# Kernel optimization log

Hardware: AMD Instinct MI355X
Metric: run time of the kernel (lower is better)

## Reference

```python
import jax, jax.numpy as jnp
import numpy as np

K = 2048      # codebook_size
D = 64        # codebook_dim
B = 32
T = 4096
W = 0.99      # codebook_loss_weight (EMA decay)
THRESH = 1.0  # discard_vec_threshold


def setup_inputs() -> dict:
    key = jax.random.key(0)
    k1, k2 = jax.random.split(key, 2)
    x = jax.random.normal(k1, (B, D, T), jnp.float32)
    codebook = jax.random.normal(k2, (K, D), jnp.float32)
    codebook_avg = codebook.copy()
    vector_usage = jnp.ones((K,), jnp.float32)
    perm = jnp.arange(B * T, dtype=jnp.int32)  # deterministic stand-in for randperm
    return dict(x=x, codebook=codebook, codebook_avg=codebook_avg,
                vector_usage=vector_usage, perm=perm)


def reference(x, codebook, codebook_avg, vector_usage, perm):
    Bv, E, Tv = x.shape
    sg = jax.lax.stop_gradient
    # preprocess: [B, E, T] -> [N, E]
    xf = jnp.transpose(x, (0, 2, 1)).reshape(-1, E)
    N = xf.shape[0]
    x_norm = jnp.linalg.norm(xf - jnp.mean(xf)) / np.sqrt(N * E)
    # squared euclidean distances [N, K]
    d = (jnp.sum(xf * xf, axis=-1, keepdims=True)
         - 2.0 * (xf @ codebook.T)
         + jnp.sum(codebook * codebook, axis=-1))
    idx = jnp.argmin(d, axis=-1)            # [N]
    fit = jnp.mean(jnp.min(d, axis=-1))
    q = codebook[idx]                       # [N, E] gather
    # --- update_codebook (torch.no_grad) ---
    cb_sum = jax.ops.segment_sum(sg(xf), idx, num_segments=K)          # onehot @ x
    counts = jax.ops.segment_sum(jnp.ones((N,), xf.dtype), idx, num_segments=K)
    new_avg = W * sg(codebook_avg) + (1.0 - W) * cb_sum
    new_usage = W * sg(vector_usage) + (1.0 - W) * counts
    keep = (new_usage >= THRESH).astype(xf.dtype)[:, None]
    random_shift = sg(xf)[perm][:K]
    new_codebook = keep * (new_avg / new_usage[:, None]) + (1.0 - keep) * random_shift
    vector_prob = counts / jnp.sum(counts)
    entropy = -jnp.sum(vector_prob * jnp.log(vector_prob + 1e-8))
    codebook_diff = jnp.linalg.norm(new_codebook - sg(codebook)) / np.sqrt(K * E)
    # --- commitment loss + straight-through ---
    commit_loss = jnp.sum((sg(q) - xf) ** 2) / (N * E)
    out = xf + sg(q - xf)
    out = jnp.transpose(out.reshape(Bv, Tv, E), (0, 2, 1))  # [B, E, T]
    return (out, commit_loss, fit, x_norm, new_codebook, new_avg, new_usage,
            entropy, codebook_diff)
```

## Files before the change

### kernel.cpp

```cpp
#include <hip/hip_runtime.h>
#include <math.h>

#define OUT_X      0
#define OUT_COMMIT 8388608
#define OUT_FIT    8388609
#define OUT_XNORM  8388610
#define OUT_NCB    8388611
#define OUT_NAVG   (8388611 + 131072)
#define OUT_NUSE   (8388611 + 262144)
#define OUT_ENT    (8388611 + 264192)
#define OUT_CBDIFF (8388611 + 264193)

#define WS_DACC    0
#define WS_COUNTS  64
#define WS_CBSUM   8256
#define WS_CURS    532544
#define WS_XN2     540736
#define WS_IDX     1065024
#define WS_CN2H    1589312
#define WS_SORTED  1597504
#define WS_CHI     2121792
#define WS_CLO     2383936
#define WS_ZERO_BYTES 532544

#define LO_SCALE   2048.0f
#define LO_INV     4.8828125e-4f

typedef _Float16 f16x8_t __attribute__((ext_vector_type(8)));
typedef float f32x16_t __attribute__((ext_vector_type(16)));

__device__ __forceinline__ void gload_lds16(const _Float16* g, _Float16* l) {
    __builtin_amdgcn_global_load_lds(
        (const __attribute__((address_space(1))) unsigned int*)(g),
        (__attribute__((address_space(3))) unsigned int*)(l), 16, 0, 0);
}

__global__ __launch_bounds__(256) void kern_prep_x(
    const float* __restrict__ x, float* __restrict__ xt,
    float* __restrict__ xn2, double* __restrict__ dacc)
{
    __shared__ __align__(16) float Xs[64][128];
    __shared__ float tmpA[4], tmpB[4];
    const int tid = threadIdx.x;
    const int n0 = blockIdx.x * 128;
    const int b = n0 >> 12, t0 = n0 & 4095;
    const float* xb = x + ((size_t)b << 18) + t0;
#pragma unroll
    for (int i = 0; i < 8; ++i) {
        int c = i * 256 + tid;
        int e = c >> 5, v4 = c & 31;
        float4 f = *(const float4*)(xb + ((size_t)e << 12) + (v4 << 2));
        *(float4*)&Xs[e][v4 << 2] = f;
    }
    __syncthreads();
    const int q = tid & 3, r0 = tid >> 2;
    float s1t = 0.f, s2t = 0.f;
#pragma unroll
    for (int h = 0; h < 2; ++h) {
        int r = r0 + (h << 6);
        float s2 = 0.f;
#pragma unroll
        for (int j = 0; j < 4; ++j) {
            int e = q * 16 + j * 4;
            float4 f = make_float4(Xs[e][r], Xs[e + 1][r], Xs[e + 2][r], Xs[e + 3][r]);
            *(float4*)(xt + (((size_t)(n0 + r)) << 6) + e) = f;
            s1t += f.x + f.y + f.z + f.w;
            s2 += f.x * f.x + f.y * f.y + f.z * f.z + f.w * f.w;
        }
        s2t += s2;
        float s2q = s2 + __shfl_xor(s2, 1, 64);
        s2q += __shfl_xor(s2q, 2, 64);
        if (q == 0) xn2[n0 + r] = s2q;
    }
    float rs = s1t, r2 = s2t;
#pragma unroll
    for (int m = 32; m >= 1; m >>= 1) {
        rs += __shfl_xor(rs, m, 64);
        r2 += __shfl_xor(r2, m, 64);
    }
    if ((tid & 63) == 0) { tmpA[tid >> 6] = rs; tmpB[tid >> 6] = r2; }
    __syncthreads();
    if (tid == 0) {
        atomicAdd(&dacc[0], (double)(tmpA[0] + tmpA[1] + tmpA[2] + tmpA[3]));
        atomicAdd(&dacc[1], (double)(tmpB[0] + tmpB[1] + tmpB[2] + tmpB[3]));
    }
}

__global__ __launch_bounds__(256) void kern_prep_cb(
    const float* __restrict__ cb, _Float16* __restrict__ chi,
    _Float16* __restrict__ clo, float* __restrict__ cn2h)
{
    __shared__ float Cs[128][68];
    const int tid = threadIdx.x;
    const int c0 = blockIdx.x * 128;
#pragma unroll
    for (int i = 0; i < 8; ++i) {
        int li = i * 256 + tid;
        int code = li >> 4, d4 = li & 15;
        float4 f = *(const float4*)(cb + (((size_t)(c0 + code)) << 6) + (d4 << 2));
        Cs[code][d4 * 4 + 0] = f.x; Cs[code][d4 * 4 + 1] = f.y;
        Cs[code][d4 * 4 + 2] = f.z; Cs[code][d4 * 4 + 3] = f.w;
    }
    __syncthreads();
    const int w = tid >> 6, lane = tid & 63;
    const int cl = (w << 5) + (lane & 31);
    const int g = lane >> 5;
    const int ktg = blockIdx.x * 4 + w;
#pragma unroll
    for (int s = 0; s < 4; ++s) {
        f16x8_t hh, ll;
#pragma unroll
        for (int i = 0; i < 8; ++i) {
            int k = 16 * s + 4 * g + (i & 3) + 8 * (i >> 2);
            float v = Cs[cl][k];
            _Float16 h = (_Float16)v;
            hh[i] = h;
            ll[i] = (_Float16)((v - (float)h) * LO_SCALE);
        }
        *(f16x8_t*)(chi + (((size_t)(ktg * 4 + s)) << 9) + lane * 8) = hh;
        *(f16x8_t*)(clo + (((size_t)(ktg * 4 + s)) << 9) + lane * 8) = ll;
    }
    if (tid < 128) {
        float s = 0.f;
#pragma unroll
        for (int k = 0; k < 64; ++k) { float v = Cs[tid][k]; s = fmaf(v, v, s); }
        cn2h[c0 + tid] = -0.5f * s;
    }
}

__global__ __launch_bounds__(256, 4) void kern_argmin_mfma(
    const float* __restrict__ xt, const float* __restrict__ cn2h,
    const _Float16* __restrict__ chi, const _Float16* __restrict__ clo,
    const float* __restrict__ xn2, int* __restrict__ idxb,
    unsigned* __restrict__ counts, double* __restrict__ dacc)
{
    __shared__ __align__(16) _Float16 Bs[2][2][8][512];
    const int tid = threadIdx.x;
    const int w = tid >> 6, lane = tid & 63;
    const int n0 = blockIdx.x * 128 + w * 32;
    const int l31 = lane & 31, g = lane >> 5;

    f16x8_t ahi[4], alo[4];
    {
        const float* xr = xt + ((size_t)(n0 + l31) << 6) + 4 * g;
#pragma unroll
        for (int s = 0; s < 4; ++s) {
            float4 p = *(const float4*)(xr + 16 * s);
            float4 q = *(const float4*)(xr + 16 * s + 8);
            float vals[8] = {p.x, p.y, p.z, p.w, q.x, q.y, q.z, q.w};
#pragma unroll
            for (int i = 0; i < 8; ++i) {
                _Float16 h = (_Float16)vals[i];
                ahi[s][i] = h;
                alo[s][i] = (_Float16)((vals[i] - (float)h) * LO_SCALE);
            }
        }
    }
    float bestm[16]; int besti[16];
#pragma unroll
    for (int r = 0; r < 16; ++r) { bestm[r] = -INFINITY; besti[r] = 0; }

#pragma unroll
    for (int j = 0; j < 4; ++j) {
        int seg = (j << 2) | w;
        int tt = seg >> 3, sh = seg & 7;
        size_t off = (((size_t)(0 * 2 + tt) * 4 + (sh >> 1)) << 9) + lane * 8;
        gload_lds16(((sh & 1) ? clo : chi) + off, &Bs[0][tt][sh][0]);
    }
    __syncthreads();
    int buf = 0;
    for (int kt2 = 0; kt2 < 32; ++kt2) {
        if (kt2 + 1 < 32) {
#pragma unroll
            for (int j = 0; j < 4; ++j) {
                int seg = (j << 2) | w;
                int tt = seg >> 3, sh = seg & 7;
                size_t off = (((size_t)(kt2 + 1) * 2 + tt) * 4 + (sh >> 1) << 9) + lane * 8;
                gload_lds16(((sh & 1) ? clo : chi) + off, &Bs[buf ^ 1][tt][sh][0]);
            }
        }
#pragma unroll
        for (int tt = 0; tt < 2; ++tt) {
            const int tg = kt2 * 2 + tt;
            float cv = cn2h[(tg << 5) + l31];
            f32x16_t am, ac;
#pragma unroll
            for (int r = 0; r < 16; ++r) { am[r] = cv; ac[r] = 0.f; }
#pragma unroll
            for (int s = 0; s < 4; ++s) {
                f16x8_t bh = *(const f16x8_t*)&Bs[buf][tt][s * 2 + 0][lane * 8];
                f16x8_t bl = *(const f16x8_t*)&Bs[buf][tt][s * 2 + 1][lane * 8];
                ac = __builtin_amdgcn_mfma_f32_32x32x16_f16(alo[s], bh, ac, 0, 0, 0);
                ac = __builtin_amdgcn_mfma_f32_32x32x16_f16(ahi[s], bl, ac, 0, 0, 0);
                am = __builtin_amdgcn_mfma_f32_32x32x16_f16(ahi[s], bh, am, 0, 0, 0);
            }
#pragma unroll
            for (int r = 0; r < 16; ++r) {
                float m = fmaf(LO_INV, ac[r], am[r]);
                if (m > bestm[r]) { bestm[r] = m; besti[r] = tg; }
            }
        }
        __syncthreads();
        buf ^= 1;
    }
    float fs = 0.f;
#pragma unroll
    for (int r = 0; r < 16; ++r) {
        float mv = bestm[r]; int mi = (besti[r] << 5) + l31;
#pragma unroll
        for (int m = 1; m < 32; m <<= 1) {
            float ov = __shfl_xor(mv, m, 64);
            int oi = __shfl_xor(mi, m, 64);
            if (ov > mv || (ov == mv && oi < mi)) { mv = ov; mi = oi; }
        }
        if (l31 == 0) {
            int row = (r & 3) + 8 * (r >> 2) + 4 * g;
            int n = n0 + row;
            idxb[n] = mi;
            atomicAdd(&counts[mi], 1u);
            fs += xn2[n] - 2.f * mv;
        }
    }
    if (l31 == 0) atomicAdd(&dacc[2], (double)fs);
}

__global__ void kern_scan(const unsigned* __restrict__ counts, unsigned* __restrict__ curs) {
    __shared__ unsigned wtot[4];
    const int tid = threadIdx.x;
    const int base = tid * 8;
    unsigned s[8]; unsigned tot = 0;
#pragma unroll
    for (int j = 0; j < 8; ++j) { s[j] = counts[base + j]; tot += s[j]; }
    unsigned v = tot;
    const int lane = tid & 63;
#pragma unroll
    for (int d = 1; d < 64; d <<= 1) {
        unsigned o = (unsigned)__shfl_up((int)v, d, 64);
        if (lane >= d) v += o;
    }
    if (lane == 63) wtot[tid >> 6] = v;
    __syncthreads();
    unsigned wbase = 0;
    for (int w = 0; w < (tid >> 6); ++w) wbase += wtot[w];
    unsigned run = wbase + v - tot;
#pragma unroll
    for (int j = 0; j < 8; ++j) { curs[base + j] = run; run += s[j]; }
}

__global__ void kern_scatter(const int* __restrict__ idxb, unsigned* __restrict__ curs,
                             unsigned* __restrict__ sorted) {
    const int n = blockIdx.x * 256 + threadIdx.x;
    int k = idxb[n];
    unsigned pos = atomicAdd(&curs[k], 1u);
    sorted[pos] = ((unsigned)k << 17) | (unsigned)n;
}

__global__ __launch_bounds__(256) void kern_chunk_reduce(
    const float* __restrict__ xt, const unsigned* __restrict__ sorted,
    float* __restrict__ cb_sum)
{
    const int tid = threadIdx.x;
    const int w = tid >> 6, lane = tid & 63;
    const int base = blockIdx.x * 256 + w * 64;
    int kcur = (int)(sorted[base] >> 17);
    float acc = 0.f;
#pragma unroll 4
    for (int it = 0; it < 16; ++it) {
        uint4 p = *(const uint4*)&sorted[base + it * 4];
        float v0 = xt[((size_t)(p.x & 0x1FFFFu) << 6) + lane];
        float v1 = xt[((size_t)(p.y & 0x1FFFFu) << 6) + lane];
        float v2 = xt[((size_t)(p.z & 0x1FFFFu) << 6) + lane];
        float v3 = xt[((size_t)(p.w & 0x1FFFFu) << 6) + lane];
        int k0 = (int)(p.x >> 17), k1 = (int)(p.y >> 17);
        int k2 = (int)(p.z >> 17), k3 = (int)(p.w >> 17);
        if (k0 != kcur) { atomicAdd(&cb_sum[(kcur << 6) + lane], acc); kcur = k0; acc = 0.f; }
        acc += v0;
        if (k1 != kcur) { atomicAdd(&cb_sum[(kcur << 6) + lane], acc); kcur = k1; acc = 0.f; }
        acc += v1;
        if (k2 != kcur) { atomicAdd(&cb_sum[(kcur << 6) + lane], acc); kcur = k2; acc = 0.f; }
        acc += v2;
        if (k3 != kcur) { atomicAdd(&cb_sum[(kcur << 6) + lane], acc); kcur = k3; acc = 0.f; }
        acc += v3;
    }
    atomicAdd(&cb_sum[(kcur << 6) + lane], acc);
}

__global__ __launch_bounds__(256) void kern_update(
    const float* __restrict__ cb_sum, const unsigned* __restrict__ counts,
    const float* __restrict__ cb, const float* __restrict__ cba,
    const float* __restrict__ usage, const int* __restrict__ perm,
    const float* __restrict__ xt, float* __restrict__ out,
    double* __restrict__ dacc)
{
    const int tid = threadIdx.x;
    const int i = blockIdx.x * 256 + tid;
    const int k = i >> 6, e = i & 63;
    float na = 0.99f * cba[i] + 0.01f * cb_sum[i];
    float nu = 0.99f * usage[k] + 0.01f * (float)counts[k];
    float ncb = (nu >= 1.0f) ? (na / nu)
                             : xt[((size_t)perm[k] << 6) + e];
    out[OUT_NAVG + i] = na;
    out[OUT_NCB + i] = ncb;
    if (e == 0) out[OUT_NUSE + k] = nu;
    float d = ncb - cb[i];
    float dd = d * d;
#pragma unroll
    for (int m = 32; m >= 1; m >>= 1) dd += __shfl_xor(dd, m, 64);
    if (e == 0) atomicAdd(&dacc[4], (double)dd);
}

__global__ __launch_bounds__(256) void kern_out(
    const float* __restrict__ x, const float* __restrict__ cb,
    const int* __restrict__ idxb, float* __restrict__ out,
    double* __restrict__ dacc) {
    __shared__ float tmp[4];
    const int tid = threadIdx.x;
    const int n0 = blockIdx.x * 256 + (tid & 63) * 4;
    const int ec = tid >> 6;
    const int b = n0 >> 12, t = n0 & 4095;
    int4 k4 = *(const int4*)(idxb + n0);
    const float* xb = x + ((size_t)b << 18) + t;
    float* ob = out + OUT_X + ((size_t)b << 18) + t;
    float cl = 0.f;
#pragma unroll
    for (int j = 0; j < 16; ++j) {
        int e = ec * 16 + j;
        float4 xv = *(const float4*)(xb + ((size_t)e << 12));
        float q0 = cb[((size_t)k4.x << 6) + e], q1 = cb[((size_t)k4.y << 6) + e];
        float q2 = cb[((size_t)k4.z << 6) + e], q3 = cb[((size_t)k4.w << 6) + e];
        float r0 = q0 - xv.x, r1 = q1 - xv.y, r2 = q2 - xv.z, r3 = q3 - xv.w;
        cl += r0 * r0 + r1 * r1 + r2 * r2 + r3 * r3;
        *(float4*)(ob + ((size_t)e << 12)) = make_float4(q0, q1, q2, q3);
    }
#pragma unroll
    for (int m = 32; m >= 1; m >>= 1) cl += __shfl_xor(cl, m, 64);
    if ((tid & 63) == 0) tmp[tid >> 6] = cl;
    __syncthreads();
    if (tid == 0) atomicAdd(&dacc[3], (double)(tmp[0] + tmp[1] + tmp[2] + tmp[3]));
}

__global__ void kern_scalars(const unsigned* __restrict__ counts,
                             const double* __restrict__ dacc, float* __restrict__ out) {
    __shared__ float tmp[4];
    __shared__ float totalSh;
    const int tid = threadIdx.x;
    float c = 0.f;
    for (int k = tid; k < 2048; k += 256) c += (float)counts[k];
#pragma unroll
    for (int m = 32; m >= 1; m >>= 1) c += __shfl_xor(c, m, 64);
    if ((tid & 63) == 0) tmp[tid >> 6] = c;
    __syncthreads();
    if (tid == 0) totalSh = tmp[0] + tmp[1] + tmp[2] + tmp[3];
    __syncthreads();
    const float total = totalSh;
    float ent = 0.f;
    for (int k = tid; k < 2048; k += 256) {
        float p = (float)counts[k] / total;
        ent -= p * logf(p + 1e-8f);
    }
#pragma unroll
    for (int m = 32; m >= 1; m >>= 1) ent += __shfl_xor(ent, m, 64);
    __syncthreads();
    if ((tid & 63) == 0) tmp[tid >> 6] = ent;
    __syncthreads();
    if (tid == 0) {
        float entropy = tmp[0] + tmp[1] + tmp[2] + tmp[3];
        out[OUT_COMMIT] = (float)(dacc[3] / 8388608.0);
        out[OUT_FIT]    = (float)(dacc[2] / 131072.0);
        double nd = 8388608.0;
        double var = dacc[1] - dacc[0] * dacc[0] / nd;
        if (var < 0.0) var = 0.0;
        out[OUT_XNORM] = (float)(sqrt(var) / sqrt(nd));
        out[OUT_ENT] = entropy;
        out[OUT_CBDIFF] = (float)(sqrt(dacc[4]) / sqrt(131072.0));
    }
}

extern "C" void kernel_launch(void* const* d_in, const int* in_sizes, int n_in,
                              void* d_out, int out_size, void* d_ws, size_t ws_size,
                              hipStream_t stream) {
    const float* x     = (const float*)d_in[0];
    const float* cb    = (const float*)d_in[1];
    const float* cba   = (const float*)d_in[2];
    const float* usage = (const float*)d_in[3];
    const int*   perm  = (const int*)d_in[4];
    float* out = (float*)d_out;
    char* ws = (char*)d_ws;
    double*    dacc   = (double*)(ws + WS_DACC);
    unsigned*  counts = (unsigned*)(ws + WS_COUNTS);
    float*     cbsum  = (float*)(ws + WS_CBSUM);
    unsigned*  curs   = (unsigned*)(ws + WS_CURS);
    float*     xn2    = (float*)(ws + WS_XN2);
    int*       idxb   = (int*)(ws + WS_IDX);
    float*     cn2h   = (float*)(ws + WS_CN2H);
    unsigned*  sorted = (unsigned*)(ws + WS_SORTED);
    _Float16*  chi    = (_Float16*)(ws + WS_CHI);
    _Float16*  clo    = (_Float16*)(ws + WS_CLO);
    float*     xt     = out + OUT_X;

    hipMemsetAsync(ws, 0, WS_ZERO_BYTES, stream);
    kern_prep_x<<<1024, 256, 0, stream>>>(x, xt, xn2, dacc);
    kern_prep_cb<<<16, 256, 0, stream>>>(cb, chi, clo, cn2h);
    kern_argmin_mfma<<<1024, 256, 0, stream>>>(xt, cn2h, chi, clo, xn2, idxb, counts, dacc);
    kern_scan<<<1, 256, 0, stream>>>(counts, curs);
    kern_scatter<<<512, 256, 0, stream>>>(idxb, curs, sorted);
    kern_chunk_reduce<<<512, 256, 0, stream>>>(xt, sorted, cbsum);
    kern_update<<<512, 256, 0, stream>>>(cbsum, counts, cb, cba, usage, perm, xt, out, dacc);
    kern_out<<<512, 256, 0, stream>>>(x, cb, idxb, out, dacc);
    kern_scalars<<<1, 256, 0, stream>>>(counts, dacc, out);
}
```

Baseline: 292.9 us.

## Process two row blocks per wave with triple-buffered codebook tiles in argmin

```diff
diff --git a/kernel.cpp b/kernel.cpp
--- a/kernel.cpp
+++ b/kernel.cpp
@@ -23,8 +23,7 @@
 #define WS_CLO     2383936
 #define WS_ZERO_BYTES 532544
 
-#define LO_SCALE   2048.0f
-#define LO_INV     4.8828125e-4f
+#define LO_SCALE5  32.0f
 
 typedef _Float16 f16x8_t __attribute__((ext_vector_type(8)));
 typedef float f32x16_t __attribute__((ext_vector_type(16)));
@@ -115,7 +114,7 @@
             float v = Cs[cl][k];
             _Float16 h = (_Float16)v;
             hh[i] = h;
-            ll[i] = (_Float16)((v - (float)h) * LO_SCALE);
+            ll[i] = (_Float16)((v - (float)h) * LO_SCALE5);
         }
         *(f16x8_t*)(chi + (((size_t)(ktg * 4 + s)) << 9) + lane * 8) = hh;
         *(f16x8_t*)(clo + (((size_t)(ktg * 4 + s)) << 9) + lane * 8) = ll;
@@ -128,21 +127,25 @@
     }
 }
 
-__global__ __launch_bounds__(256, 4) void kern_argmin_mfma(
+__global__ __launch_bounds__(256, 2) void kern_argmin_mfma(
     const float* __restrict__ xt, const float* __restrict__ cn2h,
     const _Float16* __restrict__ chi, const _Float16* __restrict__ clo,
     const float* __restrict__ xn2, int* __restrict__ idxb,
     unsigned* __restrict__ counts, double* __restrict__ dacc)
 {
-    __shared__ __align__(16) _Float16 Bs[2][2][8][512];
+    __shared__ __align__(16) _Float16 Bs[3][2][8][512];
+    __shared__ float cvs[2048];
     const int tid = threadIdx.x;
     const int w = tid >> 6, lane = tid & 63;
-    const int n0 = blockIdx.x * 128 + w * 32;
+    const int n0 = blockIdx.x * 256 + w * 64;
     const int l31 = lane & 31, g = lane >> 5;
 
-    f16x8_t ahi[4], alo[4];
-    {
-        const float* xr = xt + ((size_t)(n0 + l31) << 6) + 4 * g;
+    for (int i = tid; i < 2048; i += 256) cvs[i] = cn2h[i];
+
+    f16x8_t ahi[2][4], alo5[2][4];
+#pragma unroll
+    for (int rb = 0; rb < 2; ++rb) {
+        const float* xr = xt + ((size_t)(n0 + rb * 32 + l31) << 6) + 4 * g;
 #pragma unroll
         for (int s = 0; s < 4; ++s) {
             float4 p = *(const float4*)(xr + 16 * s);
@@ -151,76 +154,99 @@
 #pragma unroll
             for (int i = 0; i < 8; ++i) {
                 _Float16 h = (_Float16)vals[i];
-                ahi[s][i] = h;
-                alo[s][i] = (_Float16)((vals[i] - (float)h) * LO_SCALE);
-            }
-        }
-    }
-    float bestm[16]; int besti[16];
-#pragma unroll
-    for (int r = 0; r < 16; ++r) { bestm[r] = -INFINITY; besti[r] = 0; }
-
-#pragma unroll
-    for (int j = 0; j < 4; ++j) {
-        int seg = (j << 2) | w;
-        int tt = seg >> 3, sh = seg & 7;
-        size_t off = (((size_t)(0 * 2 + tt) * 4 + (sh >> 1)) << 9) + lane * 8;
-        gload_lds16(((sh & 1) ? clo : chi) + off, &Bs[0][tt][sh][0]);
-    }
-    __syncthreads();
-    int buf = 0;
-    for (int kt2 = 0; kt2 < 32; ++kt2) {
-        if (kt2 + 1 < 32) {
+                ahi[rb][s][i] = h;
+                alo5[rb][s][i] = (_Float16)((vals[i] - (float)h) * LO_SCALE5);
+            }
+        }
+    }
+    float bestm[2][16]; int besti[2][16];
+#pragma unroll
+    for (int rb = 0; rb < 2; ++rb)
+#pragma unroll
+        for (int r = 0; r < 16; ++r) { bestm[rb][r] = -INFINITY; besti[rb][r] = 0; }
+
+    __syncthreads();
+
+#pragma unroll
+    for (int kt = 0; kt < 2; ++kt)
+#pragma unroll
+        for (int j = 0; j < 4; ++j) {
+            int seg = (j << 2) | w;
+            int tt = seg >> 3, sh = seg & 7;
+            const _Float16* src = ((sh & 1) ? clo : chi)
+                + ((((size_t)(kt * 2 + tt)) * 4 + (sh >> 1)) << 9) + lane * 8;
+            gload_lds16(src, &Bs[kt][tt][sh][0]);
+        }
+
+    int cur = 0, nxt = 2;
+    for (int kt = 0; kt < 32; ++kt) {
+        if (kt < 30) asm volatile("s_waitcnt vmcnt(4)" ::: "memory");
+        else         asm volatile("s_waitcnt vmcnt(0)" ::: "memory");
+        __builtin_amdgcn_s_barrier();
+        if (kt + 2 < 32) {
 #pragma unroll
             for (int j = 0; j < 4; ++j) {
                 int seg = (j << 2) | w;
                 int tt = seg >> 3, sh = seg & 7;
-                size_t off = (((size_t)(kt2 + 1) * 2 + tt) * 4 + (sh >> 1) << 9) + lane * 8;
-                gload_lds16(((sh & 1) ? clo : chi) + off, &Bs[buf ^ 1][tt][sh][0]);
+                const _Float16* src = ((sh & 1) ? clo : chi)
+                    + ((((size_t)((kt + 2) * 2 + tt)) * 4 + (sh >> 1)) << 9) + lane * 8;
+                gload_lds16(src, &Bs[nxt][tt][sh][0]);
             }
         }
 #pragma unroll
         for (int tt = 0; tt < 2; ++tt) {
-            const int tg = kt2 * 2 + tt;
-            float cv = cn2h[(tg << 5) + l31];
-            f32x16_t am, ac;
-#pragma unroll
-            for (int r = 0; r < 16; ++r) { am[r] = cv; ac[r] = 0.f; }
+            const int tg = kt * 2 + tt;
+            f16x8_t bh[4], bl[4];
 #pragma unroll
             for (int s = 0; s < 4; ++s) {
-                f16x8_t bh = *(const f16x8_t*)&Bs[buf][tt][s * 2 + 0][lane * 8];
-                f16x8_t bl = *(const f16x8_t*)&Bs[buf][tt][s * 2 + 1][lane * 8];
-                ac = __builtin_amdgcn_mfma_f32_32x32x16_f16(alo[s], bh, ac, 0, 0, 0);
-                ac = __builtin_amdgcn_mfma_f32_32x32x16_f16(ahi[s], bl, ac, 0, 0, 0);
-                am = __builtin_amdgcn_mfma_f32_32x32x16_f16(ahi[s], bh, am, 0, 0, 0);
+                bh[s] = *(const f16x8_t*)&Bs[cur][tt][s * 2 + 0][lane * 8];
+                bl[s] = *(const f16x8_t*)&Bs[cur][tt][s * 2 + 1][lane * 8];
+            }
+            float cv = cvs[(tg << 5) + l31];
+            f32x16_t a0, a1;
+#pragma unroll
+            for (int r = 0; r < 16; ++r) { a0[r] = cv; a1[r] = cv; }
+#pragma unroll
+            for (int s = 0; s < 4; ++s) {
+                a0 = __builtin_amdgcn_mfma_f32_32x32x16_f16(ahi[0][s], bh[s], a0, 0, 0, 0);
+                a1 = __builtin_amdgcn_mfma_f32_32x32x16_f16(ahi[1][s], bh[s], a1, 0, 0, 0);
+                f16x8_t bh5 = bh[s] * (_Float16)0.03125f;
+                a0 = __builtin_amdgcn_mfma_f32_32x32x16_f16(alo5[0][s], bh5, a0, 0, 0, 0);
+                a1 = __builtin_amdgcn_mfma_f32_32x32x16_f16(alo5[1][s], bh5, a1, 0, 0, 0);
+                f16x8_t h50 = ahi[0][s] * (_Float16)0.03125f;
+                f16x8_t h51 = ahi[1][s] * (_Float16)0.03125f;
+                a0 = __builtin_amdgcn_mfma_f32_32x32x16_f16(h50, bl[s], a0, 0, 0, 0);
+                a1 = __builtin_amdgcn_mfma_f32_32x32x16_f16(h51, bl[s], a1, 0, 0, 0);
             }
 #pragma unroll
             for (int r = 0; r < 16; ++r) {
-                float m = fmaf(LO_INV, ac[r], am[r]);
-                if (m > bestm[r]) { bestm[r] = m; besti[r] = tg; }
-            }
-        }
-        __syncthreads();
-        buf ^= 1;
+                if (a0[r] > bestm[0][r]) { bestm[0][r] = a0[r]; besti[0][r] = tg; }
+                if (a1[r] > bestm[1][r]) { bestm[1][r] = a1[r]; besti[1][r] = tg; }
+            }
+        }
+        cur = (cur == 2) ? 0 : cur + 1;
+        nxt = (nxt == 2) ? 0 : nxt + 1;
     }
     float fs = 0.f;
 #pragma unroll
-    for (int r = 0; r < 16; ++r) {
-        float mv = bestm[r]; int mi = (besti[r] << 5) + l31;
-#pragma unroll
-        for (int m = 1; m < 32; m <<= 1) {
-            float ov = __shfl_xor(mv, m, 64);
-            int oi = __shfl_xor(mi, m, 64);
-            if (ov > mv || (ov == mv && oi < mi)) { mv = ov; mi = oi; }
-        }
-        if (l31 == 0) {
-            int row = (r & 3) + 8 * (r >> 2) + 4 * g;
-            int n = n0 + row;
-            idxb[n] = mi;
-            atomicAdd(&counts[mi], 1u);
-            fs += xn2[n] - 2.f * mv;
-        }
-    }
+    for (int rb = 0; rb < 2; ++rb)
+#pragma unroll
+        for (int r = 0; r < 16; ++r) {
+            float mv = bestm[rb][r]; int mi = (besti[rb][r] << 5) + l31;
+#pragma unroll
+            for (int m = 1; m < 32; m <<= 1) {
+                float ov = __shfl_xor(mv, m, 64);
+                int oi = __shfl_xor(mi, m, 64);
+                if (ov > mv || (ov == mv && oi < mi)) { mv = ov; mi = oi; }
+            }
+            if (l31 == 0) {
+                int row = (r & 3) + 8 * (r >> 2) + 4 * g;
+                int n = n0 + rb * 32 + row;
+                idxb[n] = mi;
+                atomicAdd(&counts[mi], 1u);
+                fs += xn2[n] - 2.f * mv;
+            }
+        }
     if (l31 == 0) atomicAdd(&dacc[2], (double)fs);
 }
 
@@ -401,7 +427,7 @@
     hipMemsetAsync(ws, 0, WS_ZERO_BYTES, stream);
     kern_prep_x<<<1024, 256, 0, stream>>>(x, xt, xn2, dacc);
     kern_prep_cb<<<16, 256, 0, stream>>>(cb, chi, clo, cn2h);
-    kern_argmin_mfma<<<1024, 256, 0, stream>>>(xt, cn2h, chi, clo, xn2, idxb, counts, dacc);
+    kern_argmin_mfma<<<512, 256, 0, stream>>>(xt, cn2h, chi, clo, xn2, idxb, counts, dacc);
     kern_scan<<<1, 256, 0, stream>>>(counts, curs);
     kern_scatter<<<512, 256, 0, stream>>>(idxb, curs, sorted);
     kern_chunk_reduce<<<512, 256, 0, stream>>>(xt, sorted, cbsum);
```

Result: faster. 276.4 us (-5.6%).

## Restructure argmin MFMA loop with single-barrier phases, LDS codebook norms, smaller lo scale

Applied to the files above, without the earlier changes.

```diff
diff --git a/kernel.cpp b/kernel.cpp
--- a/kernel.cpp
+++ b/kernel.cpp
@@ -23,8 +23,7 @@
 #define WS_CLO     2383936
 #define WS_ZERO_BYTES 532544
 
-#define LO_SCALE   2048.0f
-#define LO_INV     4.8828125e-4f
+#define LO_SCALE5  32.0f
 
 typedef _Float16 f16x8_t __attribute__((ext_vector_type(8)));
 typedef float f32x16_t __attribute__((ext_vector_type(16)));
@@ -115,7 +114,7 @@
             float v = Cs[cl][k];
             _Float16 h = (_Float16)v;
             hh[i] = h;
-            ll[i] = (_Float16)((v - (float)h) * LO_SCALE);
+            ll[i] = (_Float16)((v - (float)h) * LO_SCALE5);
         }
         *(f16x8_t*)(chi + (((size_t)(ktg * 4 + s)) << 9) + lane * 8) = hh;
         *(f16x8_t*)(clo + (((size_t)(ktg * 4 + s)) << 9) + lane * 8) = ll;
@@ -135,12 +134,15 @@
     unsigned* __restrict__ counts, double* __restrict__ dacc)
 {
     __shared__ __align__(16) _Float16 Bs[2][2][8][512];
+    __shared__ float cvs[2048];
     const int tid = threadIdx.x;
     const int w = tid >> 6, lane = tid & 63;
     const int n0 = blockIdx.x * 128 + w * 32;
     const int l31 = lane & 31, g = lane >> 5;
 
-    f16x8_t ahi[4], alo[4];
+    for (int i = tid; i < 2048; i += 256) cvs[i] = cn2h[i];
+
+    f16x8_t ahi[4], alo5[4];
     {
         const float* xr = xt + ((size_t)(n0 + l31) << 6) + 4 * g;
 #pragma unroll
@@ -152,7 +154,7 @@
             for (int i = 0; i < 8; ++i) {
                 _Float16 h = (_Float16)vals[i];
                 ahi[s][i] = h;
-                alo[s][i] = (_Float16)((vals[i] - (float)h) * LO_SCALE);
+                alo5[s][i] = (_Float16)((vals[i] - (float)h) * LO_SCALE5);
             }
         }
     }
@@ -160,49 +162,54 @@
 #pragma unroll
     for (int r = 0; r < 16; ++r) { bestm[r] = -INFINITY; besti[r] = 0; }
 
-#pragma unroll
-    for (int j = 0; j < 4; ++j) {
-        int seg = (j << 2) | w;
-        int tt = seg >> 3, sh = seg & 7;
-        size_t off = (((size_t)(0 * 2 + tt) * 4 + (sh >> 1)) << 9) + lane * 8;
-        gload_lds16(((sh & 1) ? clo : chi) + off, &Bs[0][tt][sh][0]);
-    }
-    __syncthreads();
-    int buf = 0;
-    for (int kt2 = 0; kt2 < 32; ++kt2) {
-        if (kt2 + 1 < 32) {
-#pragma unroll
-            for (int j = 0; j < 4; ++j) {
-                int seg = (j << 2) | w;
-                int tt = seg >> 3, sh = seg & 7;
-                size_t off = (((size_t)(kt2 + 1) * 2 + tt) * 4 + (sh >> 1) << 9) + lane * 8;
-                gload_lds16(((sh & 1) ? clo : chi) + off, &Bs[buf ^ 1][tt][sh][0]);
-            }
-        }
-#pragma unroll
-        for (int tt = 0; tt < 2; ++tt) {
-            const int tg = kt2 * 2 + tt;
-            float cv = cn2h[(tg << 5) + l31];
-            f32x16_t am, ac;
-#pragma unroll
-            for (int r = 0; r < 16; ++r) { am[r] = cv; ac[r] = 0.f; }
-#pragma unroll
-            for (int s = 0; s < 4; ++s) {
-                f16x8_t bh = *(const f16x8_t*)&Bs[buf][tt][s * 2 + 0][lane * 8];
-                f16x8_t bl = *(const f16x8_t*)&Bs[buf][tt][s * 2 + 1][lane * 8];
-                ac = __builtin_amdgcn_mfma_f32_32x32x16_f16(alo[s], bh, ac, 0, 0, 0);
-                ac = __builtin_amdgcn_mfma_f32_32x32x16_f16(ahi[s], bl, ac, 0, 0, 0);
-                am = __builtin_amdgcn_mfma_f32_32x32x16_f16(ahi[s], bh, am, 0, 0, 0);
-            }
-#pragma unroll
-            for (int r = 0; r < 16; ++r) {
-                float m = fmaf(LO_INV, ac[r], am[r]);
-                if (m > bestm[r]) { bestm[r] = m; besti[r] = tg; }
-            }
-        }
-        __syncthreads();
-        buf ^= 1;
-    }
+#define STAGE(kt_, slot_) do {                                               \
+    _Pragma("unroll")                                                        \
+    for (int j = 0; j < 4; ++j) {                                            \
+        int seg = (j << 2) | w;                                              \
+        int tt_ = seg >> 3, sh_ = seg & 7;                                   \
+        const _Float16* src = ((sh_ & 1) ? clo : chi)                        \
+            + ((((size_t)((kt_) * 2 + tt_)) * 4 + (sh_ >> 1)) << 9) + lane * 8; \
+        gload_lds16(src, &Bs[slot_][tt_][sh_][0]);                           \
+    }                                                                        \
+} while (0)
+
+#define PHASE(kt_, cs_) do {                                                 \
+    asm volatile("s_waitcnt vmcnt(0)" ::: "memory");                         \
+    __builtin_amdgcn_s_barrier();                                            \
+    if ((kt_) + 1 < 32) STAGE((kt_) + 1, (cs_) ^ 1);                         \
+    _Pragma("unroll")                                                        \
+    for (int tt = 0; tt < 2; ++tt) {                                         \
+        const int tg = (kt_) * 2 + tt;                                       \
+        float cv = cvs[(tg << 5) + l31];                                     \
+        f32x16_t am, ac;                                                     \
+        _Pragma("unroll")                                                    \
+        for (int r = 0; r < 16; ++r) { am[r] = cv; ac[r] = 0.f; }            \
+        _Pragma("unroll")                                                    \
+        for (int s = 0; s < 4; ++s) {                                        \
+            f16x8_t bh = *(const f16x8_t*)&Bs[cs_][tt][s * 2 + 0][lane * 8]; \
+            f16x8_t bl = *(const f16x8_t*)&Bs[cs_][tt][s * 2 + 1][lane * 8]; \
+            am = __builtin_amdgcn_mfma_f32_32x32x16_f16(ahi[s],  bh, am, 0, 0, 0); \
+            ac = __builtin_amdgcn_mfma_f32_32x32x16_f16(alo5[s], bh, ac, 0, 0, 0); \
+            ac = __builtin_amdgcn_mfma_f32_32x32x16_f16(ahi[s],  bl, ac, 0, 0, 0); \
+        }                                                                    \
+        _Pragma("unroll")                                                    \
+        for (int r = 0; r < 16; ++r) {                                       \
+            float m = fmaf(0.03125f, ac[r], am[r]);                          \
+            if (m > bestm[r]) { bestm[r] = m; besti[r] = tg; }               \
+        }                                                                    \
+    }                                                                        \
+} while (0)
+
+    STAGE(0, 0);
+    __syncthreads();
+
+    for (int kt = 0; kt < 32; kt += 2) {
+        PHASE(kt, 0);
+        PHASE(kt + 1, 1);
+    }
+#undef STAGE
+#undef PHASE
+
     float fs = 0.f;
 #pragma unroll
     for (int r = 0; r < 16; ++r) {
```

Measured after the change: 400.5 us. +36.8%, slower.
